# Optimization experiments

Hardware: AMD Instinct MI355X
Metric: run time of the kernel (lower is better)

The kernel has to match this reference:

```python
import jax, jax.numpy as jnp
import numpy as np

BIGNET_DIM = 1024
GROUP = 16
N_LIN = 15  # 6 blocks (last has no LN after) x 3 QLoRALinear
N_LN = 5
LORA_SCALE = 0.125  # 1/8
LN_EPS = 1e-5


def setup_inputs() -> dict:
    key = jax.random.key(0)
    ks = jax.random.split(key, 8)
    B = 8192
    x = jax.random.normal(ks[0], (B, BIGNET_DIM), dtype=jnp.float32)
    # 4-bit codes in [0, 16), group-wise fp16 scales (absmax-like, positive)
    q_w = jax.random.randint(ks[1], (N_LIN, BIGNET_DIM, BIGNET_DIM), 0, 16, dtype=jnp.int32)
    scales = (jax.random.uniform(ks[2], (N_LIN, BIGNET_DIM, BIGNET_DIM // GROUP)) * 0.05 + 0.01).astype(jnp.float16)
    biases = (jax.random.normal(ks[3], (N_LIN, BIGNET_DIM)) * 0.01).astype(jnp.float16)
    lora_A = jax.random.normal(ks[4], (N_LIN, 32, BIGNET_DIM), dtype=jnp.float32) * (1.0 / np.sqrt(BIGNET_DIM))
    # lora_B is zero-init in the module; use small random values so the LoRA path is exercised
    lora_B = jax.random.normal(ks[5], (N_LIN, BIGNET_DIM, 32), dtype=jnp.float32) * 0.01
    ln_g = jnp.ones((N_LN, BIGNET_DIM), dtype=jnp.float32)
    ln_b = jnp.zeros((N_LN, BIGNET_DIM), dtype=jnp.float32)
    return {"x": x, "q_w": q_w, "scales": scales, "biases": biases,
            "lora_A": lora_A, "lora_B": lora_B, "ln_g": ln_g, "ln_b": ln_b}


def _dequant4bit(q, scale):
    # q: [out, in] int codes in [0,16); scale: [out, in//GROUP] fp16
    # w = (q / 15 * 2 - 1) * group_scale, computed in fp16 like the torch code
    s = jnp.repeat(scale, GROUP, axis=1)  # [out, in]
    return (q.astype(jnp.float16) * jnp.float16(2.0 / 15.0) - jnp.float16(1.0)) * s


def _qlora_linear(x, q, scale, bias, A, B):
    w = _dequant4bit(q, scale)                                   # [out, in] f16
    half = jnp.dot(x.astype(jnp.float16), w.T) + bias            # f16 GEMM
    lora = jnp.dot(jnp.dot(x, A.T), B.T) * LORA_SCALE            # f32 rank-32 path
    return half.astype(jnp.float32) + lora


def _layernorm(x, g, b):
    mu = jnp.mean(x, axis=-1, keepdims=True)
    var = jnp.mean(jnp.square(x - mu), axis=-1, keepdims=True)
    return (x - mu) * jax.lax.rsqrt(var + LN_EPS) * g + b


def _forward(x, q_w, scales, biases, lora_A, lora_B, ln_g, ln_b):
    h = x
    li = 0
    for blk in range(6):
        r = h
        for j in range(3):
            r = _qlora_linear(r, q_w[li], scales[li], biases[li], lora_A[li], lora_B[li])
            li += 1
            if j < 2:
                r = jax.nn.relu(r)
        h = r + h  # block residual
        if blk < 5:
            h = _layernorm(h, ln_g[blk], ln_b[blk])
    return h


def reference(x, q_w, scales, biases, lora_A, lora_B, ln_g, ln_b):
    return _forward(x, q_w, scales, biases, lora_A, lora_B, ln_g, ln_b)
```

## Files before the change

kernel.cpp:

```cpp
#include <hip/hip_runtime.h>

typedef _Float16 f16;
typedef _Float16 f16x8 __attribute__((ext_vector_type(8)));
typedef _Float16 f16x4 __attribute__((ext_vector_type(4)));
typedef float f32x4 __attribute__((ext_vector_type(4)));

#define GLDS(gp, lp) __builtin_amdgcn_global_load_lds( \
    (__attribute__((address_space(1))) void*)(gp),     \
    (__attribute__((address_space(3))) void*)(lp), 16, 0, 0)

__global__ void detect_kernel(const unsigned short* __restrict__ sc, int* __restrict__ mode)
{
    if (threadIdx.x != 0 || blockIdx.x != 0) return;
    bool ok16 = true, okbf = true;
    for (int i = 0; i < 64; i++) {
        const unsigned short b = sc[i];
        union { unsigned short u; f16 h; } ch; ch.u = b;
        const float fv = (float)ch.h;
        if (!(fv > 0.008f && fv < 0.062f)) ok16 = false;
        union { unsigned int u; float f; } cb; cb.u = ((unsigned int)b) << 16;
        if (!(cb.f > 0.008f && cb.f < 0.062f)) okbf = false;
    }
    *mode = ok16 ? 0 : (okbf ? 1 : 2);
}

__device__ __forceinline__ float load_half_like(const void* p, int i, int mode)
{
    if (mode == 0) return (float)((const f16*)p)[i];
    if (mode == 1) {
        union { unsigned int u; float f; } c;
        c.u = ((unsigned int)((const unsigned short*)p)[i]) << 16;
        return c.f;
    }
    return ((const float*)p)[i];
}

__global__ void prep_kernel(const float* __restrict__ x, const int* __restrict__ qw,
                            const void* __restrict__ scales, const void* __restrict__ biases,
                            const float* __restrict__ lA, const float* __restrict__ lB,
                            const int* __restrict__ modep,
                            f16* __restrict__ Wdq, f16* __restrict__ A16,
                            f16* __restrict__ B16, f16* __restrict__ x16,
                            float* __restrict__ bias32)
{
    const int bid = blockIdx.x, tid = threadIdx.x;
    if (bid < 3840) {
        const int md = *modep;
        const int g = bid * 256 + tid;
        const float s = load_half_like(scales, g, md);
        const int4* qp = (const int4*)(qw + (size_t)g * 16);
        f16x8 w0, w1;
        #pragma unroll
        for (int v = 0; v < 4; v++) {
            const int4 q4 = qp[v];
            const int qs[4] = {q4.x, q4.y, q4.z, q4.w};
            #pragma unroll
            for (int j = 0; j < 4; j++) {
                f16 t = (f16)qs[j];
                t = t * (f16)(2.0f / 15.0f);
                t = t - (f16)1.0f;
                const f16 w = (f16)((float)t * s);
                if (v < 2) w0[v * 4 + j] = w; else w1[(v - 2) * 4 + j] = w;
            }
        }
        *(f16x8*)(Wdq + (size_t)g * 16) = w0;
        *(f16x8*)(Wdq + (size_t)g * 16 + 8) = w1;
    } else if (bid < 4320) {
        const int i = (bid - 3840) * 1024 + tid * 4;
        const float4 a = *(const float4*)(lA + i);
        f16x4 o = {(f16)a.x, (f16)a.y, (f16)a.z, (f16)a.w};
        *(f16x4*)(A16 + i) = o;
    } else if (bid < 4800) {
        const int i = (bid - 4320) * 1024 + tid * 4;
        const float4 a = *(const float4*)(lB + i);
        f16x4 o = {(f16)(0.125f * a.x), (f16)(0.125f * a.y),
                   (f16)(0.125f * a.z), (f16)(0.125f * a.w)};
        *(f16x4*)(B16 + i) = o;
    } else if (bid < 12992) {
        const int i = (bid - 4800) * 1024 + tid * 4;
        const float4 a = *(const float4*)(x + i);
        f16x4 o = {(f16)a.x, (f16)a.y, (f16)a.z, (f16)a.w};
        *(f16x4*)(x16 + i) = o;
    } else {
        const int md = *modep;
        const int i = (bid - 12992) * 1024 + tid * 4;
        float4 o;
        o.x = load_half_like(biases, i, md);
        o.y = load_half_like(biases, i + 1, md);
        o.z = load_half_like(biases, i + 2, md);
        o.w = load_half_like(biases, i + 3, md);
        *(float4*)(bias32 + i) = o;
    }
}

__global__ __launch_bounds__(256, 2)
void layer_kernel(const f16* __restrict__ X16, const f16* __restrict__ W,
                  const f16* __restrict__ AL, const f16* __restrict__ BL,
                  const float* __restrict__ biasL, const float* __restrict__ resid,
                  float* __restrict__ out32, f16* __restrict__ out16, int do_relu)
{
    __shared__ __align__(16) f16 lds[36864];

    const int tid  = threadIdx.x;
    const int lane = tid & 63;
    const int wv   = tid >> 6;
    const int wy   = wv >> 1, wx = wv & 1;
    const int by   = blockIdx.x & 63;
    const int bx   = blockIdx.x >> 6;
    const int row0 = by << 7;
    const int col0 = bx << 7;

    const int lr = lane >> 3;
    const int lk = (lane & 7) << 3;
    const int m15 = lane & 15;
    const int q8  = (lane >> 4) << 3;

    f32x4 acc[4][4] = {};
    f32x4 tacc[2][2] = {};

    auto stage = [&](int kt, f16* buf) {
        const int kb = kt << 6;
        #pragma unroll
        for (int i = 0; i < 4; i++) {
            GLDS(X16 + (size_t)(row0 + wv * 32 + i * 8 + lr) * 1024 + kb + lk,
                 buf + (wv * 32 + i * 8) * 64);
            GLDS(W + (size_t)(col0 + wv * 32 + i * 8 + lr) * 1024 + kb + lk,
                 buf + 8192 + (wv * 32 + i * 8) * 64);
        }
        GLDS(AL + (size_t)(wv * 8 + lr) * 1024 + kb + lk, buf + 16384 + (wv * 8) * 64);
    };

    stage(0, lds);

    for (int kt = 0; kt < 16; kt++) {
        const f16* cur = lds + (kt & 1) * 18432;
        __syncthreads();
        const f16* sA = cur;
        const f16* sB = cur + 8192;
        const f16* sL = cur + 16384;

        f16x8 af[2][4], bf[2][4], lf[2][2];
        #pragma unroll
        for (int s = 0; s < 2; s++) {
            const int kk = s * 32 + q8;
            #pragma unroll
            for (int mi = 0; mi < 4; mi++)
                af[s][mi] = *(const f16x8*)(sA + (wy * 64 + mi * 16 + m15) * 64 + kk);
            #pragma unroll
            for (int ni = 0; ni < 4; ni++)
                bf[s][ni] = *(const f16x8*)(sB + (wx * 64 + ni * 16 + m15) * 64 + kk);
            #pragma unroll
            for (int pi = 0; pi < 2; pi++)
                lf[s][pi] = *(const f16x8*)(sL + (pi * 16 + m15) * 64 + kk);
        }

        if (kt < 15) stage(kt + 1, lds + ((kt + 1) & 1) * 18432);

        #pragma unroll
        for (int s = 0; s < 2; s++) {
            #pragma unroll
            for (int mi = 0; mi < 4; mi++)
                #pragma unroll
                for (int ni = 0; ni < 4; ni++)
                    acc[mi][ni] = __builtin_amdgcn_mfma_f32_16x16x32_f16(af[s][mi], bf[s][ni], acc[mi][ni], 0, 0, 0);
            #pragma unroll
            for (int mi = 0; mi < 2; mi++)
                #pragma unroll
                for (int pi = 0; pi < 2; pi++)
                    tacc[mi][pi] = __builtin_amdgcn_mfma_f32_16x16x32_f16(af[s][2 * wx + mi], lf[s][pi], tacc[mi][pi], 0, 0, 0);
        }
    }

    __syncthreads();
    float* Tl = (float*)lds;
    const int q4 = (lane >> 4) << 2;
    {
        #pragma unroll
        for (int mi = 0; mi < 2; mi++)
            #pragma unroll
            for (int pi = 0; pi < 2; pi++)
                #pragma unroll
                for (int r = 0; r < 4; r++)
                    Tl[(wy * 64 + wx * 32 + mi * 16 + q4 + r) * 32 + pi * 16 + m15] = tacc[mi][pi][r];
    }
    __syncthreads();

    f16x8 tf[4];
    #pragma unroll
    for (int mi = 0; mi < 4; mi++) {
        const float* tp = Tl + (wy * 64 + mi * 16 + m15) * 32 + q8;
        f16x8 v;
        #pragma unroll
        for (int j = 0; j < 8; j++) v[j] = (f16)tp[j];
        tf[mi] = v;
    }
    f16x8 bfr[4]; float bb[4];
    #pragma unroll
    for (int ni = 0; ni < 4; ni++) {
        const int colg = col0 + wx * 64 + ni * 16 + m15;
        bfr[ni] = *(const f16x8*)(BL + (size_t)colg * 32 + q8);
        bb[ni] = biasL[colg];
    }
    #pragma unroll
    for (int mi = 0; mi < 4; mi++)
        #pragma unroll
        for (int ni = 0; ni < 4; ni++) {
            #pragma unroll
            for (int r = 0; r < 4; r++)
                acc[mi][ni][r] += bb[ni];
            acc[mi][ni] = __builtin_amdgcn_mfma_f32_16x16x32_f16(tf[mi], bfr[ni], acc[mi][ni], 0, 0, 0);
        }

    __syncthreads();
    if (out16) {
        f16* ot = lds;
        #pragma unroll
        for (int mi = 0; mi < 4; mi++)
            #pragma unroll
            for (int ni = 0; ni < 4; ni++)
                #pragma unroll
                for (int r = 0; r < 4; r++) {
                    float v = acc[mi][ni][r];
                    if (do_relu) v = fmaxf(v, 0.0f);
                    ot[(wy * 64 + mi * 16 + q4 + r) * 136 + wx * 64 + ni * 16 + m15] = (f16)v;
                }
        __syncthreads();
        const int rr = tid >> 4;
        const int cc = (tid & 15) << 3;
        #pragma unroll
        for (int it = 0; it < 8; it++) {
            const int r = it * 16 + rr;
            const f16x8 v = *(const f16x8*)(ot + r * 136 + cc);
            *(f16x8*)(out16 + (size_t)(row0 + r) * 1024 + col0 + cc) = v;
        }
    } else {
        float* otf = (float*)lds;
        const int rr = tid >> 5;
        const int cc = (tid & 31) << 2;
        #pragma unroll
        for (int half = 0; half < 2; half++) {
            if (wy == half) {
                #pragma unroll
                for (int mi = 0; mi < 4; mi++)
                    #pragma unroll
                    for (int ni = 0; ni < 4; ni++)
                        #pragma unroll
                        for (int r = 0; r < 4; r++)
                            otf[(mi * 16 + q4 + r) * 140 + wx * 64 + ni * 16 + m15] = acc[mi][ni][r];
            }
            __syncthreads();
            #pragma unroll
            for (int it = 0; it < 8; it++) {
                const int r = it * 8 + rr;
                f32x4 v = *(const f32x4*)(otf + r * 140 + cc);
                const size_t gidx = (size_t)(row0 + half * 64 + r) * 1024 + col0 + cc;
                const f32x4 rs = *(const f32x4*)(resid + gidx);
                v += rs;
                *(f32x4*)(out32 + gidx) = v;
            }
            if (half == 0) __syncthreads();
        }
    }
}

__global__ void ln_kernel(float* __restrict__ h, f16* __restrict__ h16,
                          const float* __restrict__ g, const float* __restrict__ b)
{
    const int row = blockIdx.x, tid = threadIdx.x;
    float* hp = h + (size_t)row * 1024;
    const int c = tid * 4;
    const float4 v = *(const float4*)(hp + c);
    float s = v.x + v.y + v.z + v.w;
    #pragma unroll
    for (int off = 32; off > 0; off >>= 1) s += __shfl_down(s, off);
    __shared__ float r1[4], r2[4];
    const int wv = tid >> 6, lane = tid & 63;
    if (lane == 0) r1[wv] = s;
    __syncthreads();
    const float mu = (r1[0] + r1[1] + r1[2] + r1[3]) * (1.0f / 1024.0f);
    const float dx = v.x - mu, dy = v.y - mu, dz = v.z - mu, dw = v.w - mu;
    float s2 = dx * dx + dy * dy + dz * dz + dw * dw;
    #pragma unroll
    for (int off = 32; off > 0; off >>= 1) s2 += __shfl_down(s2, off);
    if (lane == 0) r2[wv] = s2;
    __syncthreads();
    const float var = (r2[0] + r2[1] + r2[2] + r2[3]) * (1.0f / 1024.0f);
    const float rs = 1.0f / sqrtf(var + 1e-5f);
    float4 o;
    o.x = dx * rs * g[c]     + b[c];
    o.y = dy * rs * g[c + 1] + b[c + 1];
    o.z = dz * rs * g[c + 2] + b[c + 2];
    o.w = dw * rs * g[c + 3] + b[c + 3];
    *(float4*)(hp + c) = o;
    f16x4 o16 = {(f16)o.x, (f16)o.y, (f16)o.z, (f16)o.w};
    *(f16x4*)(h16 + (size_t)row * 1024 + c) = o16;
}

extern "C" void kernel_launch(void* const* d_in, const int* in_sizes, int n_in,
                              void* d_out, int out_size, void* d_ws, size_t ws_size,
                              hipStream_t stream)
{
    const float* x      = (const float*)d_in[0];
    const int*   qw     = (const int*)d_in[1];
    const void*  scales = d_in[2];
    const void*  biases = d_in[3];
    const float* lA     = (const float*)d_in[4];
    const float* lB     = (const float*)d_in[5];
    const float* lng    = (const float*)d_in[6];
    const float* lnb    = (const float*)d_in[7];
    float* out = (float*)d_out;

    char* ws = (char*)d_ws;
    int*   mode   = (int*)(ws);
    float* bias32 = (float*)(ws + 64);
    f16* Wdq = (f16*)(ws + 65536u);
    f16* A16 = (f16*)(ws + 31522816u);
    f16* B16 = (f16*)(ws + 32505856u);
    f16* fA  = (f16*)(ws + 33488896u);
    f16* fB  = (f16*)(ws + 50266112u);
    float* h32 = out;

    detect_kernel<<<1, 64, 0, stream>>>((const unsigned short*)scales, mode);
    prep_kernel<<<13007, 256, 0, stream>>>(x, qw, scales, biases, lA, lB, mode,
                                           Wdq, A16, B16, fA, bias32);

    int li = 0;
    for (int blk = 0; blk < 6; blk++) {
        const float* resid = (blk == 0) ? x : h32;
        for (int j = 0; j < 3; j++, li++) {
            const int wl = li < 15 ? li : 14;
            const f16* in16 = (j == 1) ? fB : fA;
            f16* o16 = (j == 0) ? fB : (j == 1 ? fA : (f16*)nullptr);
            float* o32 = nullptr;
            const float* rz = nullptr;
            if (j == 2) { o32 = h32; rz = resid; }
            layer_kernel<<<512, 256, 0, stream>>>(in16,
                Wdq + (size_t)wl * 1048576,
                A16 + (size_t)wl * 32768,
                B16 + (size_t)wl * 32768,
                bias32 + (size_t)wl * 1024,
                rz, o32, o16, j < 2 ? 1 : 0);
        }
        if (blk < 5)
            ln_kernel<<<8192, 256, 0, stream>>>(h32, fA, lng + blk * 1024, lnb + blk * 1024);
    }
}
```

Baseline: 1.486 ms.

## Stage GEMM tiles through registers with XOR-swizzled LDS layout

Replaces direct global-to-LDS async loads with global loads into registers that are written to LDS after the MFMA block. The LDS writes use an XOR swizzle on the 16-byte chunk index so the fragment reads avoid bank conflicts. The LoRA intermediate buffer is padded to a row stride of 33 floats for the same reason. This costs extra VGPRs for the staged registers and adds a scheduling barrier, which may reduce occupancy or overlap.

```diff
diff --git a/kernel.cpp b/kernel.cpp
--- a/kernel.cpp
+++ b/kernel.cpp
@@ -4,10 +4,6 @@
 typedef _Float16 f16x8 __attribute__((ext_vector_type(8)));
 typedef _Float16 f16x4 __attribute__((ext_vector_type(4)));
 typedef float f32x4 __attribute__((ext_vector_type(4)));
-
-#define GLDS(gp, lp) __builtin_amdgcn_global_load_lds( \
-    (__attribute__((address_space(1))) void*)(gp),     \
-    (__attribute__((address_space(3))) void*)(lp), 16, 0, 0)
 
 __global__ void detect_kernel(const unsigned short* __restrict__ sc, int* __restrict__ mode)
 {
@@ -111,30 +107,45 @@
     const int col0 = bx << 7;
 
     const int lr = lane >> 3;
-    const int lk = (lane & 7) << 3;
+    const int pc = lane & 7;
+    const int gk = pc << 3;
+    const int wc = ((pc ^ lr) << 3);
+
     const int m15 = lane & 15;
-    const int q8  = (lane >> 4) << 3;
+    const int q2  = lane >> 4;
+    const int sw  = m15 & 7;
+    const int po0 = ((q2 ^ sw) << 3);
+    const int po1 = (((4 + q2) ^ sw) << 3);
+    const int q8  = q2 << 3;
 
     f32x4 acc[4][4] = {};
     f32x4 tacc[2][2] = {};
-
-    auto stage = [&](int kt, f16* buf) {
+    f16x8 rx[4], rw[4], rl;
+
+    auto gload = [&](int kt) {
         const int kb = kt << 6;
         #pragma unroll
         for (int i = 0; i < 4; i++) {
-            GLDS(X16 + (size_t)(row0 + wv * 32 + i * 8 + lr) * 1024 + kb + lk,
-                 buf + (wv * 32 + i * 8) * 64);
-            GLDS(W + (size_t)(col0 + wv * 32 + i * 8 + lr) * 1024 + kb + lk,
-                 buf + 8192 + (wv * 32 + i * 8) * 64);
-        }
-        GLDS(AL + (size_t)(wv * 8 + lr) * 1024 + kb + lk, buf + 16384 + (wv * 8) * 64);
+            rx[i] = *(const f16x8*)(X16 + (size_t)(row0 + wv * 32 + i * 8 + lr) * 1024 + kb + gk);
+            rw[i] = *(const f16x8*)(W   + (size_t)(col0 + wv * 32 + i * 8 + lr) * 1024 + kb + gk);
+        }
+        rl = *(const f16x8*)(AL + (size_t)(wv * 8 + lr) * 1024 + kb + gk);
     };
-
-    stage(0, lds);
+    auto swrite = [&](f16* buf) {
+        #pragma unroll
+        for (int i = 0; i < 4; i++) {
+            *(f16x8*)(buf + (wv * 32 + i * 8 + lr) * 64 + wc) = rx[i];
+            *(f16x8*)(buf + 8192 + (wv * 32 + i * 8 + lr) * 64 + wc) = rw[i];
+        }
+        *(f16x8*)(buf + 16384 + (wv * 8 + lr) * 64 + wc) = rl;
+    };
+
+    gload(0);
+    swrite(lds);
 
     for (int kt = 0; kt < 16; kt++) {
+        __syncthreads();
         const f16* cur = lds + (kt & 1) * 18432;
-        __syncthreads();
         const f16* sA = cur;
         const f16* sB = cur + 8192;
         const f16* sL = cur + 16384;
@@ -142,19 +153,19 @@
         f16x8 af[2][4], bf[2][4], lf[2][2];
         #pragma unroll
         for (int s = 0; s < 2; s++) {
-            const int kk = s * 32 + q8;
+            const int po = s ? po1 : po0;
             #pragma unroll
             for (int mi = 0; mi < 4; mi++)
-                af[s][mi] = *(const f16x8*)(sA + (wy * 64 + mi * 16 + m15) * 64 + kk);
+                af[s][mi] = *(const f16x8*)(sA + (wy * 64 + mi * 16 + m15) * 64 + po);
             #pragma unroll
             for (int ni = 0; ni < 4; ni++)
-                bf[s][ni] = *(const f16x8*)(sB + (wx * 64 + ni * 16 + m15) * 64 + kk);
+                bf[s][ni] = *(const f16x8*)(sB + (wx * 64 + ni * 16 + m15) * 64 + po);
             #pragma unroll
             for (int pi = 0; pi < 2; pi++)
-                lf[s][pi] = *(const f16x8*)(sL + (pi * 16 + m15) * 64 + kk);
-        }
-
-        if (kt < 15) stage(kt + 1, lds + ((kt + 1) & 1) * 18432);
+                lf[s][pi] = *(const f16x8*)(sL + (pi * 16 + m15) * 64 + po);
+        }
+
+        if (kt < 15) gload(kt + 1);
 
         #pragma unroll
         for (int s = 0; s < 2; s++) {
@@ -169,6 +180,9 @@
                 for (int pi = 0; pi < 2; pi++)
                     tacc[mi][pi] = __builtin_amdgcn_mfma_f32_16x16x32_f16(af[s][2 * wx + mi], lf[s][pi], tacc[mi][pi], 0, 0, 0);
         }
+
+        __builtin_amdgcn_sched_barrier(0);
+        if (kt < 15) swrite(lds + ((kt + 1) & 1) * 18432);
     }
 
     __syncthreads();
@@ -181,14 +195,14 @@
             for (int pi = 0; pi < 2; pi++)
                 #pragma unroll
                 for (int r = 0; r < 4; r++)
-                    Tl[(wy * 64 + wx * 32 + mi * 16 + q4 + r) * 32 + pi * 16 + m15] = tacc[mi][pi][r];
+                    Tl[(wy * 64 + wx * 32 + mi * 16 + q4 + r) * 33 + pi * 16 + m15] = tacc[mi][pi][r];
     }
     __syncthreads();
 
     f16x8 tf[4];
     #pragma unroll
     for (int mi = 0; mi < 4; mi++) {
-        const float* tp = Tl + (wy * 64 + mi * 16 + m15) * 32 + q8;
+        const float* tp = Tl + (wy * 64 + mi * 16 + m15) * 33 + q8;
         f16x8 v;
         #pragma unroll
         for (int j = 0; j < 8; j++) v[j] = (f16)tp[j];
```

New measurement: 1.466 ms. No clear change (-1.3%).
